# Performance work log

Hardware: AMD Instinct MI355X
Metric: run time of the kernel (lower is better)

Reference implementation:

```python
import jax, jax.numpy as jnp
import numpy as np
from jax import lax

B, N, C = 4, 8000, 91
IMG_H, IMG_W = 800, 1333
WX, WY, WW, WH = 10.0, 10.0, 5.0, 5.0
BBOX_XFORM_CLIP = float(np.log(1000.0 / 16.0))
SCORE_THRESH = 0.05
NMS_THRESH = 0.5
DET_PER_IMG = 100
MIN_SIZE = 0.01
NEG = jnp.float32(-1e30)


def setup_inputs() -> dict:
    key = jax.random.key(0)
    k1, k2, k3 = jax.random.split(key, 3)
    class_logits = jax.random.normal(k1, (B * N, C), dtype=jnp.float32) * 2.0
    box_regression = jax.random.normal(k2, (B * N, C * 4), dtype=jnp.float32) * 0.5
    p = jax.random.uniform(k3, (B, N, 4), dtype=jnp.float32)
    x1 = p[..., 0] * (IMG_W - 150.0)
    y1 = p[..., 1] * (IMG_H - 150.0)
    x2 = x1 + 4.0 + p[..., 2] * 140.0
    y2 = y1 + 4.0 + p[..., 3] * 140.0
    proposals = jnp.stack([x1, y1, x2, y2], axis=-1)
    return {"class_logits": class_logits, "box_regression": box_regression, "proposals": proposals}


def _decode(rel, props):
    # torchvision BoxCoder.decode with weights (10,10,5,5). rel: [N, C*4], props: [N, 4]
    w = props[:, 2] - props[:, 0]
    h = props[:, 3] - props[:, 1]
    cx = props[:, 0] + 0.5 * w
    cy = props[:, 1] + 0.5 * h
    rel = rel.reshape(rel.shape[0], -1, 4)  # [N, C, 4]
    dx = rel[..., 0] / WX
    dy = rel[..., 1] / WY
    dw = jnp.minimum(rel[..., 2] / WW, BBOX_XFORM_CLIP)
    dh = jnp.minimum(rel[..., 3] / WH, BBOX_XFORM_CLIP)
    pcx = dx * w[:, None] + cx[:, None]
    pcy = dy * h[:, None] + cy[:, None]
    pw = jnp.exp(dw) * w[:, None]
    ph = jnp.exp(dh) * h[:, None]
    return jnp.stack([pcx - 0.5 * pw, pcy - 0.5 * ph, pcx + 0.5 * pw, pcy + 0.5 * ph], axis=-1)


def _iou_one_vs_all(b, bs):
    # b: [4], bs: [M, 4]
    ix1 = jnp.maximum(b[0], bs[:, 0])
    iy1 = jnp.maximum(b[1], bs[:, 1])
    ix2 = jnp.minimum(b[2], bs[:, 2])
    iy2 = jnp.minimum(b[3], bs[:, 3])
    inter = jnp.clip(ix2 - ix1, 0.0) * jnp.clip(iy2 - iy1, 0.0)
    a1 = (b[2] - b[0]) * (b[3] - b[1])
    a2 = (bs[:, 2] - bs[:, 0]) * (bs[:, 3] - bs[:, 1])
    return inter / (a1 + a2 - inter)


def _process_image(logits, rel, props):
    # logits: [N, C], rel: [N, C*4], props: [N, 4]
    boxes = _decode(rel, props)  # [N, C, 4]
    # clip_boxes_to_image
    boxes = jnp.stack([
        jnp.clip(boxes[..., 0], 0.0, IMG_W),
        jnp.clip(boxes[..., 1], 0.0, IMG_H),
        jnp.clip(boxes[..., 2], 0.0, IMG_W),
        jnp.clip(boxes[..., 3], 0.0, IMG_H),
    ], axis=-1)
    scores = jax.nn.softmax(logits, axis=-1)
    # drop background class 0 and flatten to [N*(C-1)] candidates
    boxes = boxes[:, 1:, :].reshape(-1, 4)
    scores = scores[:, 1:].reshape(-1)
    labels = jnp.broadcast_to(jnp.arange(1, C, dtype=jnp.int32), (N, C - 1)).reshape(-1)
    bw = boxes[:, 2] - boxes[:, 0]
    bh = boxes[:, 3] - boxes[:, 1]
    valid = (scores > SCORE_THRESH) & (bw >= MIN_SIZE) & (bh >= MIN_SIZE)
    # batched_nms: offset boxes per class so cross-class boxes never overlap
    sg_boxes = lax.stop_gradient(boxes)
    sg_scores = lax.stop_gradient(jnp.where(valid, scores, NEG))
    off = labels.astype(boxes.dtype) * (sg_boxes.max() + 1.0)
    nb = sg_boxes + off[:, None]

    def step(s, _):
        i = jnp.argmax(s)
        si = s[i]
        iou = _iou_one_vs_all(nb[i], nb)
        s2 = jnp.where(iou > NMS_THRESH, NEG, s).at[i].set(NEG)
        return s2, (i, si > NEG / 2)

    _, (idxs, ok) = lax.scan(step, sg_scores, None, length=DET_PER_IMG)
    det_boxes = jnp.where(ok[:, None], boxes[idxs], 0.0)
    det_scores = jnp.where(ok, scores[idxs], 0.0)
    det_labels = jnp.where(ok, labels[idxs], 0)
    return det_boxes, det_scores, det_labels


def reference(class_logits, box_regression, proposals):
    logits = class_logits.reshape(B, N, C)
    rel = box_regression.reshape(B, N, C * 4)
    boxes, scores, labels = jax.vmap(_process_image)(logits, rel, proposals)
    return boxes, scores, labels
```

## Files before the change

kernel.cpp:

```cpp
#include <hip/hip_runtime.h>
#include <math.h>

#pragma clang fp contract(off)

#define NB 4
#define NN 8000
#define NC 91
#define CM1 90
#define CAP 2048
#define ACAP 256
#define ATHR 192
#define GCAP 65536
#define RPB 32
#define BPI (NN / RPB)
#define LCAP 608
#define GWB 16

#define CNT_W(b) ((b) * 64)
#define MAX_W(b) (256 + (b) * 64)
#define CNTA_W(b) (512 + (b) * 64)
#define CNTR_W(b) (768 + (b) * 64)
#define HIST_OFF 1024
#define ZERO_WORDS (HIST_OFF + NB * 1024)
#define GBOX_OFF 5120
#define GSC_OFF (GBOX_OFF + NB * GCAP * 4)
#define GOID_OFF (GSC_OFF + NB * GCAP)
#define ABOX_OFF (GOID_OFF + NB * GCAP)
#define AKEY_OFF (ABOX_OFF + NB * ACAP * 4)
#define RBOX_OFF (AKEY_OFF + NB * ACAP * 2)
#define RKEY_OFF (RBOX_OFF + NB * CAP * 4)

__global__ void init_kernel(int* ws_i) {
  const int i = blockIdx.x * 256 + threadIdx.x;
  if (i < ZERO_WORDS) ws_i[i] = 0;
}

__global__ void __launch_bounds__(256) cand_kernel(const float* __restrict__ logits,
                                                   const float* __restrict__ rel,
                                                   const float* __restrict__ props,
                                                   int* __restrict__ ws_i,
                                                   float* __restrict__ ws_f) {
  const int blk = blockIdx.x;
  const int b = blk / BPI;
  const int ib = blk - b * BPI;
  const int t = threadIdx.x;
  const int L = t & 15;
  const int grp = t >> 4;
  const int lane = t & 63;

  __shared__ float sbx[LCAP][4];
  __shared__ float ssb[LCAP];
  __shared__ int soidb[LCAP];
  __shared__ int lhist[1024];
  __shared__ int scnt;
  __shared__ int smaxs;
  __shared__ int sgbase;
  for (int j = t; j < 1024; j += 256) lhist[j] = 0;
  if (t == 0) { scnt = 0; smaxs = 0; }
  __syncthreads();

  int tmax = 0;

  for (int i = 0; i < RPB / 16; ++i) {
    const int row = b * NN + ib * RPB + i * 16 + grp;
    const float* lp = logits + (size_t)row * NC;

    float lv[6];
#pragma unroll
    for (int j = 0; j < 6; ++j) {
      const int k = L + 16 * j;
      lv[j] = (k < NC) ? lp[k] : -INFINITY;
    }
    float tm0 = fmax(lv[0], lv[4]), tm1 = fmax(lv[1], lv[5]);
    float tm2 = lv[2], tm3 = lv[3];
    float um0 = fmax(tm0, tm2), um1 = fmax(tm1, tm3);
    float m = fmax(um0, um1);
    m = fmaxf(m, __shfl_xor(m, 8));
    m = fmaxf(m, __shfl_xor(m, 4));
    m = fmaxf(m, __shfl_xor(m, 2));
    m = fmaxf(m, __shfl_xor(m, 1));

    float ev[6];
#pragma unroll
    for (int j = 0; j < 6; ++j) {
      const int k = L + 16 * j;
      ev[j] = (k < NC) ? expf(lv[j] - m) : 0.0f;
    }
    float ts0 = ev[0] + ev[4], ts1 = ev[1] + ev[5];
    float ts2 = ev[2], ts3 = ev[3];
    float us0 = ts0 + ts2, us1 = ts1 + ts3;
    float sum = us0 + us1;
    sum += __shfl_xor(sum, 8);
    sum += __shfl_xor(sum, 4);
    sum += __shfl_xor(sum, 2);
    sum += __shfl_xor(sum, 1);

    const float4 p = reinterpret_cast<const float4*>(props)[row];
    const float w = p.z - p.x, h = p.w - p.y;
    const float cx = p.x + 0.5f * w, cy = p.y + 0.5f * h;

#pragma unroll
    for (int j = 0; j < 6; ++j) {
      const int c = L + 16 * j;
      if (c >= 1 && c < NC) {
        const float4 r = reinterpret_cast<const float4*>(rel)[(size_t)row * NC + c];
        const float dx = r.x / 10.0f, dy = r.y / 10.0f;
        const float dw = fminf(r.z / 5.0f, 4.135166556742356f);
        const float dh = fminf(r.w / 5.0f, 4.135166556742356f);
        const float pcx = dx * w + cx, pcy = dy * h + cy;
        const float pw = expf(dw) * w, ph = expf(dh) * h;
        float x1 = pcx - 0.5f * pw, y1 = pcy - 0.5f * ph;
        float x2 = pcx + 0.5f * pw, y2 = pcy + 0.5f * ph;
        x1 = fminf(fmaxf(x1, 0.0f), 1333.0f);
        y1 = fminf(fmaxf(y1, 0.0f), 800.0f);
        x2 = fminf(fmaxf(x2, 0.0f), 1333.0f);
        y2 = fminf(fmaxf(y2, 0.0f), 800.0f);
        const float score = ev[j] / sum;
        const float localmax = fmaxf(fmaxf(x1, y1), fmaxf(x2, y2));
        tmax = max(tmax, __float_as_int(localmax));
        const float bw = x2 - x1, bh = y2 - y1;
        if ((score > 0.05f) && (bw >= 0.01f) && (bh >= 0.01f)) {
          const int slot = atomicAdd(&scnt, 1);
          sbx[slot][0] = x1; sbx[slot][1] = y1;
          sbx[slot][2] = x2; sbx[slot][3] = y2;
          ssb[slot] = score;
          soidb[slot] = (row - b * NN) * CM1 + (c - 1);
          int bi = (int)(__float_as_uint(score) >> 16) - 15360;
          bi = min(max(bi, 0), 1023);
          atomicAdd(&lhist[bi], 1);
        }
      }
    }
  }
  tmax = max(tmax, __shfl_xor(tmax, 32));
  tmax = max(tmax, __shfl_xor(tmax, 16));
  tmax = max(tmax, __shfl_xor(tmax, 8));
  tmax = max(tmax, __shfl_xor(tmax, 4));
  tmax = max(tmax, __shfl_xor(tmax, 2));
  tmax = max(tmax, __shfl_xor(tmax, 1));
  if (lane == 0) atomicMax(&smaxs, tmax);
  __syncthreads();
  const int n = scnt;
  if (t == 0) {
    sgbase = atomicAdd(&ws_i[CNT_W(b)], n);
    atomicMax(&ws_i[MAX_W(b)], smaxs);
  }
  __syncthreads();
  const int gb = sgbase;
  for (int j = t; j < n; j += 256) {
    const int pos = gb + j;
    if (pos < GCAP) {
      reinterpret_cast<float4*>(ws_f + GBOX_OFF)[b * GCAP + pos] =
          make_float4(sbx[j][0], sbx[j][1], sbx[j][2], sbx[j][3]);
      ws_f[GSC_OFF + b * GCAP + pos] = ssb[j];
      ws_i[GOID_OFF + b * GCAP + pos] = soidb[j];
    }
  }
  for (int j = t; j < 1024; j += 256) {
    const int v = lhist[j];
    if (v) atomicAdd(&ws_i[HIST_OFF + b * 1024 + j], v);
  }
}

__global__ void __launch_bounds__(256) gather_kernel(int* __restrict__ ws_i,
                                                     float* __restrict__ ws_f) {
  const int b = blockIdx.x / GWB, sub = blockIdx.x % GWB;
  const int t = threadIdx.x;
  __shared__ int seg[256];
  __shared__ int best1, best2;
  __shared__ int lidxA[ACAP];
  __shared__ int lidxR[CAP];
  __shared__ int cA, cR, baseA, baseR;

  const int* H = ws_i + HIST_OFF + b * 1024;
  const int h0 = H[4 * t + 0], h1 = H[4 * t + 1];
  const int h2 = H[4 * t + 2], h3 = H[4 * t + 3];
  seg[t] = h0 + h1 + h2 + h3;
  if (t == 0) { best1 = 1024; best2 = 1024; cA = 0; cR = 0; }
  __syncthreads();
  for (int off = 1; off < 256; off <<= 1) {
    const int v = (t + off < 256) ? seg[t + off] : 0;
    __syncthreads();
    seg[t] += v;
    __syncthreads();
  }
  const int higher = (t < 255) ? seg[t + 1] : 0;
  {
    int A = higher; int cnd = 0x7FFFFFFF;
    A += h3; if (A <= CAP) cnd = 4 * t + 3;
    A += h2; if (A <= CAP) cnd = 4 * t + 2;
    A += h1; if (A <= CAP) cnd = 4 * t + 1;
    A += h0; if (A <= CAP) cnd = 4 * t + 0;
    if (cnd != 0x7FFFFFFF) atomicMin(&best1, cnd);
  }
  {
    int A = higher; int cnd = 0x7FFFFFFF;
    A += h3; if (A <= ATHR) cnd = 4 * t + 3;
    A += h2; if (A <= ATHR) cnd = 4 * t + 2;
    A += h1; if (A <= ATHR) cnd = 4 * t + 1;
    A += h0; if (A <= ATHR) cnd = 4 * t + 0;
    if (cnd != 0x7FFFFFFF) atomicMin(&best2, cnd);
  }
  __syncthreads();
  const int tk = best1, tk2 = best2;

  int M = ws_i[CNT_W(b)];
  if (M > GCAP) M = GCAP;
  const float* gsc = ws_f + GSC_OFF + (size_t)b * GCAP;
  const int* goid = ws_i + GOID_OFF + (size_t)b * GCAP;
  const float4* gbox = reinterpret_cast<const float4*>(ws_f + GBOX_OFF) + (size_t)b * GCAP;
  float4* abox = reinterpret_cast<float4*>(ws_f + ABOX_OFF) + (size_t)b * ACAP;
  unsigned long long* akey = reinterpret_cast<unsigned long long*>(ws_i + AKEY_OFF) + (size_t)b * ACAP;
  float4* rbox = reinterpret_cast<float4*>(ws_f + RBOX_OFF) + (size_t)b * CAP;
  unsigned long long* rkey = reinterpret_cast<unsigned long long*>(ws_i + RKEY_OFF) + (size_t)b * CAP;

  for (int j = sub * 256 + t; j < M; j += GWB * 256) {
    const float s = gsc[j];
    int bi = (int)(__float_as_uint(s) >> 16) - 15360;
    bi = min(max(bi, 0), 1023);
    if (bi >= tk2) {
      const int p = atomicAdd(&cA, 1);
      if (p < ACAP) lidxA[p] = j;
    } else if (bi >= tk) {
      const int p = atomicAdd(&cR, 1);
      if (p < CAP) lidxR[p] = j;
    }
  }
  __syncthreads();
  const int nAb = min(cA, ACAP), nRb = min(cR, CAP);
  if (t == 0) {
    baseA = atomicAdd(&ws_i[CNTA_W(b)], nAb);
    baseR = atomicAdd(&ws_i[CNTR_W(b)], nRb);
  }
  __syncthreads();
  for (int k = t; k < nAb; k += 256) {
    const int j = lidxA[k];
    const int pos = baseA + k;
    if (pos < ACAP) {
      abox[pos] = gbox[j];
      akey[pos] = ((unsigned long long)(__float_as_uint(gsc[j]) | 0x80000000u) << 32) |
                  (unsigned)(0xFFFFFFFFu - (unsigned)goid[j]);
    }
  }
  for (int k = t; k < nRb; k += 256) {
    const int j = lidxR[k];
    const int pos = baseR + k;
    if (pos < CAP) {
      rbox[pos] = gbox[j];
      rkey[pos] = ((unsigned long long)(__float_as_uint(gsc[j]) | 0x80000000u) << 32) |
                  (unsigned)(0xFFFFFFFFu - (unsigned)goid[j]);
    }
  }
}

__global__ void __launch_bounds__(256) nms_kernel(const int* __restrict__ ws_i,
                                                  const float* __restrict__ ws_f,
                                                  float* __restrict__ out) {
  const int b = blockIdx.x;
  const int t = threadIdx.x;
  const int lane = t & 63;
  __shared__ __align__(16) char sm[57344];
  unsigned long long* akey = (unsigned long long*)sm;
  float4* abox = (float4*)(sm + 2048);
  unsigned long long* skeyS = (unsigned long long*)(sm + 6144);
  float4* sboxS = (float4*)(sm + 8192);
  int* slblS = (int*)(sm + 12288);
  unsigned long long* suppm = (unsigned long long*)(sm + 13312);
  unsigned long long* rkeyS = (unsigned long long*)sm;
  float4* rboxS = (float4*)(sm + 16384);
  int* rlblS = (int*)(sm + 49152);
  __shared__ float4 selbox[100];
  __shared__ unsigned long long selkey[100];
  __shared__ int sellbl[100];
  __shared__ int snacc;

  const int nA = min(ws_i[CNTA_W(b)], ACAP);
  const int nR = min(ws_i[CNTR_W(b)], CAP);
  const float maxp1 = __int_as_float(ws_i[MAX_W(b)]) + 1.0f;
  const float4* gA = reinterpret_cast<const float4*>(ws_f + ABOX_OFF) + (size_t)b * ACAP;
  const unsigned long long* gAk =
      reinterpret_cast<const unsigned long long*>(ws_i + AKEY_OFF) + (size_t)b * ACAP;

  akey[t] = (t < nA) ? gAk[t] : 0ull;
  if (t < nA) abox[t] = gA[t];
  skeyS[t] = 0ull;
  __syncthreads();

  {
    const unsigned long long kj = akey[t];
    if (kj != 0ull) {
      int rank = 0;
#pragma unroll 16
      for (int i = 0; i < ACAP; ++i) rank += (akey[i] > kj) ? 1 : 0;
      skeyS[rank] = kj;
      sboxS[rank] = abox[t];
      const unsigned oid = 0xFFFFFFFFu - (unsigned)(kj & 0xFFFFFFFFull);
      slblS[rank] = (int)(oid % 90u) + 1;
    }
  }
  __syncthreads();

  {
    const int i = t;
    unsigned long long r0 = 0, r1 = 0, r2 = 0, r3 = 0;
    if (i < nA) {
      const int li = slblS[i];
      const float4 bi = sboxS[i];
      const float oi = (float)li * maxp1;
      const float n0 = bi.x + oi, n1 = bi.y + oi;
      const float n2 = bi.z + oi, n3 = bi.w + oi;
      const float a1 = (n2 - n0) * (n3 - n1);
      for (int j = i + 1; j < nA; ++j) {
        if (slblS[j] == li) {
          const float4 bj = sboxS[j];
          const float q0 = bj.x + oi, q1 = bj.y + oi;
          const float q2 = bj.z + oi, q3 = bj.w + oi;
          const float ix1 = fmaxf(n0, q0), iy1 = fmaxf(n1, q1);
          const float ix2 = fminf(n2, q2), iy2 = fminf(n3, q3);
          const float inter = fmaxf(ix2 - ix1, 0.0f) * fmaxf(iy2 - iy1, 0.0f);
          const float a2 = (q2 - q0) * (q3 - q1);
          const float iou = inter / ((a1 + a2) - inter);
          if (iou > 0.5f) {
            if (j < 64) r0 |= 1ull << j;
            else if (j < 128) r1 |= 1ull << (j - 64);
            else if (j < 192) r2 |= 1ull << (j - 128);
            else r3 |= 1ull << (j - 192);
          }
        }
      }
    }
    suppm[i * 4 + 0] = r0; suppm[i * 4 + 1] = r1;
    suppm[i * 4 + 2] = r2; suppm[i * 4 + 3] = r3;
  }
  __syncthreads();

  unsigned long long m0 = 0, m1 = 0, m2 = 0, m3 = 0;
  int cnt = 0;
  int mypos = -1;
#define NMS_CHUNK(W, MW)                                              \
  if (cnt < 100) {                                                    \
    for (int jj = 0; jj < 64; ++jj) {                                 \
      const int j = (W) * 64 + jj;                                    \
      if (j >= nA || cnt == 100) break;                               \
      const unsigned long long s0 = suppm[j * 4 + 0];                 \
      const unsigned long long s1 = suppm[j * 4 + 1];                 \
      const unsigned long long s2 = suppm[j * 4 + 2];                 \
      const unsigned long long s3 = suppm[j * 4 + 3];                 \
      if (!((MW >> jj) & 1ull)) {                                     \
        if (cnt == t) mypos = j;                                      \
        ++cnt;                                                        \
        m0 |= s0; m1 |= s1; m2 |= s2; m3 |= s3;                       \
      }                                                               \
    }                                                                 \
  }
  NMS_CHUNK(0, m0)
  NMS_CHUNK(1, m1)
  NMS_CHUNK(2, m2)
  NMS_CHUNK(3, m3)
#undef NMS_CHUNK

  if (cnt >= 100 || nR == 0) {
    const int nf = min(cnt, 100);
    if (t < 100) {
      float o0 = 0.f, o1 = 0.f, o2 = 0.f, o3 = 0.f, sc = 0.f, lb = 0.f;
      if (t < nf) {
        const float4 v = sboxS[mypos];
        o0 = v.x; o1 = v.y; o2 = v.z; o3 = v.w;
        sc = __uint_as_float((unsigned)(skeyS[mypos] >> 32) & 0x7FFFFFFFu);
        lb = (float)slblS[mypos];
      }
      float* ob = out + ((size_t)b * 100 + t) * 4;
      ob[0] = o0; ob[1] = o1; ob[2] = o2; ob[3] = o3;
      out[NB * 100 * 4 + b * 100 + t] = sc;
      out[NB * 100 * 4 + NB * 100 + b * 100 + t] = lb;
    }
    return;
  }

  float A0x = 0.f, A0y = 0.f, A0z = 0.f, A0w = 0.f; int L0 = -1;
  float A1x = 0.f, A1y = 0.f, A1z = 0.f, A1w = 0.f; int L1 = -1;
  int nacc = 0;

  if (t < 64) {
    unsigned long long k0 = skeyS[0], k1 = skeyS[1];
    float4 b0 = sboxS[0], b1 = sboxS[1];
    int l0 = slblS[0], l1 = slblS[1];
    for (int j = 0; j < ACAP; ++j) {
      if (k0 == 0ull) break;
      const int jp = j + 2;
      unsigned long long k2 = 0ull;
      float4 b2 = make_float4(0.f, 0.f, 0.f, 0.f);
      int l2 = 0;
      if (jp < ACAP) { k2 = skeyS[jp]; b2 = sboxS[jp]; l2 = slblS[jp]; }
      const float oi = (float)l0 * maxp1;
      const float q0 = b0.x + oi, q1 = b0.y + oi;
      const float q2 = b0.z + oi, q3 = b0.w + oi;
      const float a2 = (q2 - q0) * (q3 - q1);
      bool sup = false;
      if (L0 == l0) {
        const float n0 = A0x + oi, n1 = A0y + oi, n2 = A0z + oi, n3 = A0w + oi;
        const float a1 = (n2 - n0) * (n3 - n1);
        const float ix1 = fmaxf(n0, q0), iy1 = fmaxf(n1, q1);
        const float ix2 = fminf(n2, q2), iy2 = fminf(n3, q3);
        const float inter = fmaxf(ix2 - ix1, 0.0f) * fmaxf(iy2 - iy1, 0.0f);
        const float iou = inter / ((a1 + a2) - inter);
        sup = (iou > 0.5f);
      }
      if (L1 == l0) {
        const float n0 = A1x + oi, n1 = A1y + oi, n2 = A1z + oi, n3 = A1w + oi;
        const float a1 = (n2 - n0) * (n3 - n1);
        const float ix1 = fmaxf(n0, q0), iy1 = fmaxf(n1, q1);
        const float ix2 = fminf(n2, q2), iy2 = fminf(n3, q3);
        const float inter = fmaxf(ix2 - ix1, 0.0f) * fmaxf(iy2 - iy1, 0.0f);
        const float iou = inter / ((a1 + a2) - inter);
        sup = sup || (iou > 0.5f);
      }
      if (!__any(sup ? 1 : 0)) {
        if (nacc < 64) {
          if (lane == nacc) { A0x = b0.x; A0y = b0.y; A0z = b0.z; A0w = b0.w; L0 = l0; }
        } else {
          if (lane == nacc - 64) { A1x = b0.x; A1y = b0.y; A1z = b0.z; A1w = b0.w; L1 = l0; }
        }
        if (lane == 0) { selbox[nacc] = b0; selkey[nacc] = k0; sellbl[nacc] = l0; }
        ++nacc;
        if (nacc == 100) break;
      }
      k0 = k1; b0 = b1; l0 = l1;
      k1 = k2; b1 = b2; l1 = l2;
    }
    if (lane == 0) snacc = nacc;
  }
  __syncthreads();

  if (snacc < 100 && nR > 0) {
    const float4* gR = reinterpret_cast<const float4*>(ws_f + RBOX_OFF) + (size_t)b * CAP;
    const unsigned long long* gRk =
        reinterpret_cast<const unsigned long long*>(ws_i + RKEY_OFF) + (size_t)b * CAP;
    for (int j = t; j < CAP; j += 256) {
      const unsigned long long k = (j < nR) ? gRk[j] : 0ull;
      rkeyS[j] = k;
      if (j < nR) {
        rboxS[j] = gR[j];
        const unsigned oid = 0xFFFFFFFFu - (unsigned)(k & 0xFFFFFFFFull);
        rlblS[j] = (int)(oid % 90u) + 1;
      }
    }
    __syncthreads();
    if (t < 64) {
      while (nacc < 100) {
        unsigned long long mk = 0ull; int mi = 0;
        for (int j = lane; j < nR; j += 64) {
          const unsigned long long k = rkeyS[j];
          if (k > mk) { mk = k; mi = j; }
        }
        for (int mm = 1; mm < 64; mm <<= 1) {
          const unsigned long long ok = __shfl_xor(mk, mm);
          const int om = __shfl_xor(mi, mm);
          if (ok > mk) { mk = ok; mi = om; }
        }
        if (mk == 0ull) break;
        if (lane == 0) rkeyS[mi] = 0ull;
        __asm__ volatile("s_waitcnt lgkmcnt(0)" ::: "memory");
        const int lbl = rlblS[mi];
        const float4 bb = rboxS[mi];
        const float oi = (float)lbl * maxp1;
        const float q0 = bb.x + oi, q1 = bb.y + oi;
        const float q2 = bb.z + oi, q3 = bb.w + oi;
        const float a2 = (q2 - q0) * (q3 - q1);
        bool sup = false;
        if (L0 == lbl) {
          const float n0 = A0x + oi, n1 = A0y + oi, n2 = A0z + oi, n3 = A0w + oi;
          const float a1 = (n2 - n0) * (n3 - n1);
          const float ix1 = fmaxf(n0, q0), iy1 = fmaxf(n1, q1);
          const float ix2 = fminf(n2, q2), iy2 = fminf(n3, q3);
          const float inter = fmaxf(ix2 - ix1, 0.0f) * fmaxf(iy2 - iy1, 0.0f);
          const float iou = inter / ((a1 + a2) - inter);
          sup = (iou > 0.5f);
        }
        if (L1 == lbl) {
          const float n0 = A1x + oi, n1 = A1y + oi, n2 = A1z + oi, n3 = A1w + oi;
          const float a1 = (n2 - n0) * (n3 - n1);
          const float ix1 = fmaxf(n0, q0), iy1 = fmaxf(n1, q1);
          const float ix2 = fminf(n2, q2), iy2 = fminf(n3, q3);
          const float inter = fmaxf(ix2 - ix1, 0.0f) * fmaxf(iy2 - iy1, 0.0f);
          const float iou = inter / ((a1 + a2) - inter);
          sup = sup || (iou > 0.5f);
        }
        if (!__any(sup ? 1 : 0)) {
          if (nacc < 64) {
            if (lane == nacc) { A0x = bb.x; A0y = bb.y; A0z = bb.z; A0w = bb.w; L0 = lbl; }
          } else {
            if (lane == nacc - 64) { A1x = bb.x; A1y = bb.y; A1z = bb.z; A1w = bb.w; L1 = lbl; }
          }
          if (lane == 0) { selbox[nacc] = bb; selkey[nacc] = mk; sellbl[nacc] = lbl; }
          ++nacc;
        }
      }
      if (lane == 0) snacc = nacc;
    }
    __syncthreads();
  }

  const int nf = snacc;
  for (int k2 = t; k2 < 100; k2 += 256) {
    float o0 = 0.f, o1 = 0.f, o2 = 0.f, o3 = 0.f, sc = 0.f, lb = 0.f;
    if (k2 < nf) {
      const float4 v = selbox[k2];
      o0 = v.x; o1 = v.y; o2 = v.z; o3 = v.w;
      sc = __uint_as_float((unsigned)(selkey[k2] >> 32) & 0x7FFFFFFFu);
      lb = (float)sellbl[k2];
    }
    float* ob = out + ((size_t)b * 100 + k2) * 4;
    ob[0] = o0; ob[1] = o1; ob[2] = o2; ob[3] = o3;
    out[NB * 100 * 4 + b * 100 + k2] = sc;
    out[NB * 100 * 4 + NB * 100 + b * 100 + k2] = lb;
  }
}

extern "C" void kernel_launch(void* const* d_in, const int* in_sizes, int n_in,
                              void* d_out, int out_size, void* d_ws, size_t ws_size,
                              hipStream_t stream) {
  const float* logits = (const float*)d_in[0];
  const float* rel = (const float*)d_in[1];
  const float* props = (const float*)d_in[2];
  float* out = (float*)d_out;
  int* ws_i = (int*)d_ws;
  float* ws_f = (float*)d_ws;

  init_kernel<<<(ZERO_WORDS + 255) / 256, 256, 0, stream>>>(ws_i);
  cand_kernel<<<NB * BPI, 256, 0, stream>>>(logits, rel, props, ws_i, ws_f);
  gather_kernel<<<NB * GWB, 256, 0, stream>>>(ws_i, ws_f);
  nms_kernel<<<NB, 256, 0, stream>>>(ws_i, ws_f, out);
}
```

Before: 82.50 us.

## Split NMS into parallel IoU-matrix kernel and single-wave greedy kernel

```diff
diff --git a/kernel.cpp b/kernel.cpp
--- a/kernel.cpp
+++ b/kernel.cpp
@@ -15,6 +15,7 @@
 #define BPI (NN / RPB)
 #define LCAP 608
 #define GWB 16
+#define MWB 4
 
 #define CNT_W(b) ((b) * 64)
 #define MAX_W(b) (256 + (b) * 64)
@@ -29,6 +30,7 @@
 #define AKEY_OFF (ABOX_OFF + NB * ACAP * 4)
 #define RBOX_OFF (AKEY_OFF + NB * ACAP * 2)
 #define RKEY_OFF (RBOX_OFF + NB * CAP * 4)
+#define MTX_OFF (RKEY_OFF + NB * CAP * 2)
 
 __global__ void init_kernel(int* ws_i) {
   const int i = blockIdx.x * 256 + threadIdx.x;
@@ -253,9 +255,72 @@
   }
 }
 
-__global__ void __launch_bounds__(256) nms_kernel(const int* __restrict__ ws_i,
-                                                  const float* __restrict__ ws_f,
-                                                  float* __restrict__ out) {
+__global__ void __launch_bounds__(256) matrix_kernel(const int* __restrict__ ws_i,
+                                                     const float* __restrict__ ws_f,
+                                                     int* __restrict__ ws_mtx) {
+  const int b = blockIdx.x / MWB, sub = blockIdx.x % MWB;
+  const int t = threadIdx.x;
+  __shared__ unsigned long long akey[ACAP];
+  __shared__ float4 abox[ACAP];
+  __shared__ float4 sboxS[ACAP];
+  __shared__ int slblS[ACAP];
+
+  const int nA = min(ws_i[CNTA_W(b)], ACAP);
+  const float maxp1 = __int_as_float(ws_i[MAX_W(b)]) + 1.0f;
+  const float4* gA = reinterpret_cast<const float4*>(ws_f + ABOX_OFF) + (size_t)b * ACAP;
+  const unsigned long long* gAk =
+      reinterpret_cast<const unsigned long long*>(ws_i + AKEY_OFF) + (size_t)b * ACAP;
+
+  akey[t] = (t < nA) ? gAk[t] : 0ull;
+  if (t < nA) abox[t] = gA[t];
+  sboxS[t] = make_float4(0.f, 0.f, 0.f, 0.f);
+  slblS[t] = -1;
+  __syncthreads();
+  {
+    const unsigned long long kj = akey[t];
+    if (kj != 0ull) {
+      int rank = 0;
+#pragma unroll 16
+      for (int i = 0; i < ACAP; ++i) rank += (akey[i] > kj) ? 1 : 0;
+      sboxS[rank] = abox[t];
+      const unsigned oid = 0xFFFFFFFFu - (unsigned)(kj & 0xFFFFFFFFull);
+      slblS[rank] = (int)(oid % 90u) + 1;
+    }
+  }
+  __syncthreads();
+
+  const int i = sub * 64 + (t >> 2);
+  const int q = t & 3;
+  const int li = slblS[i];
+  const float4 bi = sboxS[i];
+  const float oi = (float)li * maxp1;
+  const float n0 = bi.x + oi, n1 = bi.y + oi;
+  const float n2 = bi.z + oi, n3 = bi.w + oi;
+  const float a1 = (n2 - n0) * (n3 - n1);
+  unsigned long long r = 0;
+#pragma unroll 8
+  for (int k = 0; k < 64; ++k) {
+    const int j = q * 64 + k;
+    const int lj = slblS[j];
+    const float4 bj = sboxS[j];
+    const float q0 = bj.x + oi, q1 = bj.y + oi;
+    const float q2 = bj.z + oi, q3 = bj.w + oi;
+    const float ix1 = fmaxf(n0, q0), iy1 = fmaxf(n1, q1);
+    const float ix2 = fminf(n2, q2), iy2 = fminf(n3, q3);
+    const float inter = fmaxf(ix2 - ix1, 0.0f) * fmaxf(iy2 - iy1, 0.0f);
+    const float a2 = (q2 - q0) * (q3 - q1);
+    const float iou = inter / ((a1 + a2) - inter);
+    const bool hit = (j > i) & (lj == li) & (iou > 0.5f);
+    r |= hit ? (1ull << k) : 0ull;
+  }
+  unsigned long long* mtx =
+      reinterpret_cast<unsigned long long*>(ws_mtx + MTX_OFF) + (size_t)b * 1024;
+  mtx[i * 4 + q] = r;
+}
+
+__global__ void __launch_bounds__(256) greedy_kernel(const int* __restrict__ ws_i,
+                                                     const float* __restrict__ ws_f,
+                                                     float* __restrict__ out) {
   const int b = blockIdx.x;
   const int t = threadIdx.x;
   const int lane = t & 63;
@@ -272,6 +337,8 @@
   __shared__ float4 selbox[100];
   __shared__ unsigned long long selkey[100];
   __shared__ int sellbl[100];
+  __shared__ int selpos[100];
+  __shared__ int s_cnt;
   __shared__ int snacc;
 
   const int nA = min(ws_i[CNTA_W(b)], ACAP);
@@ -280,12 +347,15 @@
   const float4* gA = reinterpret_cast<const float4*>(ws_f + ABOX_OFF) + (size_t)b * ACAP;
   const unsigned long long* gAk =
       reinterpret_cast<const unsigned long long*>(ws_i + AKEY_OFF) + (size_t)b * ACAP;
+  const unsigned long long* mtx =
+      reinterpret_cast<const unsigned long long*>(ws_i + MTX_OFF) + (size_t)b * 1024;
 
   akey[t] = (t < nA) ? gAk[t] : 0ull;
   if (t < nA) abox[t] = gA[t];
   skeyS[t] = 0ull;
-  __syncthreads();
-
+  sboxS[t] = make_float4(0.f, 0.f, 0.f, 0.f);
+  slblS[t] = -1;
+  __syncthreads();
   {
     const unsigned long long kj = akey[t];
     if (kj != 0ull) {
@@ -298,72 +368,58 @@
       slblS[rank] = (int)(oid % 90u) + 1;
     }
   }
-  __syncthreads();
-
-  {
-    const int i = t;
-    unsigned long long r0 = 0, r1 = 0, r2 = 0, r3 = 0;
-    if (i < nA) {
-      const int li = slblS[i];
-      const float4 bi = sboxS[i];
-      const float oi = (float)li * maxp1;
-      const float n0 = bi.x + oi, n1 = bi.y + oi;
-      const float n2 = bi.z + oi, n3 = bi.w + oi;
-      const float a1 = (n2 - n0) * (n3 - n1);
-      for (int j = i + 1; j < nA; ++j) {
-        if (slblS[j] == li) {
-          const float4 bj = sboxS[j];
-          const float q0 = bj.x + oi, q1 = bj.y + oi;
-          const float q2 = bj.z + oi, q3 = bj.w + oi;
-          const float ix1 = fmaxf(n0, q0), iy1 = fmaxf(n1, q1);
-          const float ix2 = fminf(n2, q2), iy2 = fminf(n3, q3);
-          const float inter = fmaxf(ix2 - ix1, 0.0f) * fmaxf(iy2 - iy1, 0.0f);
-          const float a2 = (q2 - q0) * (q3 - q1);
-          const float iou = inter / ((a1 + a2) - inter);
-          if (iou > 0.5f) {
-            if (j < 64) r0 |= 1ull << j;
-            else if (j < 128) r1 |= 1ull << (j - 64);
-            else if (j < 192) r2 |= 1ull << (j - 128);
-            else r3 |= 1ull << (j - 192);
-          }
-        }
-      }
-    }
-    suppm[i * 4 + 0] = r0; suppm[i * 4 + 1] = r1;
-    suppm[i * 4 + 2] = r2; suppm[i * 4 + 3] = r3;
-  }
-  __syncthreads();
-
-  unsigned long long m0 = 0, m1 = 0, m2 = 0, m3 = 0;
-  int cnt = 0;
-  int mypos = -1;
-#define NMS_CHUNK(W, MW)                                              \
-  if (cnt < 100) {                                                    \
-    for (int jj = 0; jj < 64; ++jj) {                                 \
-      const int j = (W) * 64 + jj;                                    \
-      if (j >= nA || cnt == 100) break;                               \
-      const unsigned long long s0 = suppm[j * 4 + 0];                 \
-      const unsigned long long s1 = suppm[j * 4 + 1];                 \
-      const unsigned long long s2 = suppm[j * 4 + 2];                 \
-      const unsigned long long s3 = suppm[j * 4 + 3];                 \
-      if (!((MW >> jj) & 1ull)) {                                     \
-        if (cnt == t) mypos = j;                                      \
-        ++cnt;                                                        \
-        m0 |= s0; m1 |= s1; m2 |= s2; m3 |= s3;                       \
-      }                                                               \
-    }                                                                 \
-  }
-  NMS_CHUNK(0, m0)
-  NMS_CHUNK(1, m1)
-  NMS_CHUNK(2, m2)
-  NMS_CHUNK(3, m3)
+#pragma unroll
+  for (int j2 = 0; j2 < 4; ++j2) suppm[j2 * 256 + t] = mtx[j2 * 256 + t];
+  __syncthreads();
+
+  if (t < 64) {
+    unsigned long long m0 = 0, m1 = 0, m2 = 0, m3 = 0;
+    int cnt = 0;
+    int mypos0 = 0, mypos1 = 0;
+#define NMS_CHUNK(W, MW)                                                  \
+    if (cnt < 100 && (W)*64 < nA) {                                       \
+      for (int base = 0; base < 64 && cnt < 100; base += 8) {             \
+        unsigned long long sr0[8], sr1[8], sr2[8], sr3[8];                \
+        _Pragma("unroll")                                                 \
+        for (int k = 0; k < 8; ++k) {                                     \
+          const int j = (W) * 64 + base + k;                              \
+          sr0[k] = suppm[j * 4 + 0];                                      \
+          sr1[k] = suppm[j * 4 + 1];                                      \
+          sr2[k] = suppm[j * 4 + 2];                                      \
+          sr3[k] = suppm[j * 4 + 3];                                      \
+        }                                                                 \
+        _Pragma("unroll")                                                 \
+        for (int k = 0; k < 8; ++k) {                                     \
+          const int j = (W) * 64 + base + k;                              \
+          const bool acc =                                                \
+              (j < nA) && (cnt < 100) && !((MW >> (base + k)) & 1ull);    \
+          if (acc) {                                                      \
+            if (cnt == lane) mypos0 = j;                                  \
+            if (cnt == 64 + lane) mypos1 = j;                             \
+            ++cnt;                                                        \
+            m0 |= sr0[k]; m1 |= sr1[k]; m2 |= sr2[k]; m3 |= sr3[k];       \
+          }                                                               \
+        }                                                                 \
+      }                                                                   \
+    }
+    NMS_CHUNK(0, m0)
+    NMS_CHUNK(1, m1)
+    NMS_CHUNK(2, m2)
+    NMS_CHUNK(3, m3)
 #undef NMS_CHUNK
+    selpos[lane] = mypos0;
+    if (lane < 36) selpos[64 + lane] = mypos1;
+    if (lane == 0) s_cnt = cnt;
+  }
+  __syncthreads();
+  const int cnt = s_cnt;
 
   if (cnt >= 100 || nR == 0) {
     const int nf = min(cnt, 100);
     if (t < 100) {
       float o0 = 0.f, o1 = 0.f, o2 = 0.f, o3 = 0.f, sc = 0.f, lb = 0.f;
       if (t < nf) {
+        const int mypos = selpos[t];
         const float4 v = sboxS[mypos];
         o0 = v.x; o1 = v.y; o2 = v.z; o3 = v.w;
         sc = __uint_as_float((unsigned)(skeyS[mypos] >> 32) & 0x7FFFFFFFu);
@@ -530,5 +586,6 @@
   init_kernel<<<(ZERO_WORDS + 255) / 256, 256, 0, stream>>>(ws_i);
   cand_kernel<<<NB * BPI, 256, 0, stream>>>(logits, rel, props, ws_i, ws_f);
   gather_kernel<<<NB * GWB, 256, 0, stream>>>(ws_i, ws_f);
-  nms_kernel<<<NB, 256, 0, stream>>>(ws_i, ws_f, out);
+  matrix_kernel<<<NB * MWB, 256, 0, stream>>>(ws_i, ws_f, ws_i);
+  greedy_kernel<<<NB, 256, 0, stream>>>(ws_i, ws_f, out);
 }
```

Measured after the change: 71.54 us. 1.15x faster.
